# Kernel optimization log

Hardware: AMD Instinct MI355X
Metric: run time of the kernel (lower is better)

## Reference

```python
import jax, jax.numpy as jnp
import numpy as np

V, B, T, D, L, H = 32000, 2, 2048, 1024, 4, 16
HD = D // H            # 64
HID = int(2 * D * 4 / 3)  # 2730 (SwiGLU hidden, computed in BinaryMLP)
EPS = 1e-6


def setup_inputs() -> dict:
    key = jax.random.key(0)
    ks = jax.random.split(key, 16)
    s = 0.02
    return {
        'emb': jax.random.normal(ks[0], (V, D), jnp.float32) * s,
        'Wq':  jax.random.normal(ks[1], (L, D, D), jnp.float32) * s,
        'Wk':  jax.random.normal(ks[2], (L, D, D), jnp.float32) * s,
        'Wv':  jax.random.normal(ks[3], (L, D, D), jnp.float32) * s,
        'Wo':  jax.random.normal(ks[4], (L, D, D), jnp.float32) * s,
        'W1':  jax.random.normal(ks[5], (L, HID, D), jnp.float32) * s,
        'W3':  jax.random.normal(ks[6], (L, HID, D), jnp.float32) * s,
        'W2':  jax.random.normal(ks[7], (L, D, HID), jnp.float32) * s,
        'g1':  jnp.ones((L, D), jnp.float32),
        'g2':  jnp.ones((L, D), jnp.float32),
        'gf':  jnp.ones((D,), jnp.float32),
        'Wlm': jax.random.normal(ks[8], (V, D), jnp.float32) * s,
        'idx': jax.random.randint(ks[9], (B, T), 0, V, jnp.int64),
    }


def bitnet_quant(w):
    # BitNet b1.58: gamma = mean(|W|); ternarize then rescale (STE: identity grad)
    gamma = jnp.maximum(jnp.mean(jnp.abs(w)), 1e-5)
    wq = jnp.clip(jnp.round(w / gamma), -1.0, 1.0) * gamma
    return w + jax.lax.stop_gradient(wq - w)


def rmsnorm(x, g):
    return x * jax.lax.rsqrt(jnp.mean(x * x, axis=-1, keepdims=True) + EPS) * g


def rope_tables(t_len):
    inv_freq = 1.0 / (10000.0 ** (jnp.arange(0, HD, 2, dtype=jnp.float32) / HD))
    t = jnp.arange(t_len, dtype=jnp.float32)
    freqs = jnp.einsum('i,j->ij', t, inv_freq)       # [T, HD/2]
    emb = jnp.concatenate([freqs, freqs], axis=-1)    # [T, HD]
    return jnp.cos(emb), jnp.sin(emb)


def rotate_half(x):
    x1, x2 = x[..., : HD // 2], x[..., HD // 2:]
    return jnp.concatenate([-x2, x1], axis=-1)


def forward(emb, Wq, Wk, Wv, Wo, W1, W2, W3, g1, g2, gf, Wlm, idx):
    x = emb[idx]                                      # [B,T,D]
    cos, sin = rope_tables(T)                         # [T,HD]
    cos = cos[None, None]; sin = sin[None, None]      # [1,1,T,HD]
    causal = jnp.tril(jnp.ones((T, T), bool))[None, None]
    scale = 1.0 / np.sqrt(HD)

    for l in range(L):
        # --- attention ---
        h = rmsnorm(x, g1[l])
        q = jnp.einsum('btd,ed->bte', h, bitnet_quant(Wq[l]))
        k = jnp.einsum('btd,ed->bte', h, bitnet_quant(Wk[l]))
        v = jnp.einsum('btd,ed->bte', h, bitnet_quant(Wv[l]))
        q = q.reshape(B, T, H, HD).transpose(0, 2, 1, 3)  # [B,H,T,HD]
        k = k.reshape(B, T, H, HD).transpose(0, 2, 1, 3)
        v = v.reshape(B, T, H, HD).transpose(0, 2, 1, 3)
        q = q * cos + rotate_half(q) * sin
        k = k * cos + rotate_half(k) * sin
        att = jnp.einsum('bhqd,bhkd->bhqk', q, k) * scale
        att = jnp.where(causal, att, -jnp.inf)
        att = jax.nn.softmax(att, axis=-1)
        y = jnp.einsum('bhqk,bhkd->bhqd', att, v)
        y = y.transpose(0, 2, 1, 3).reshape(B, T, D)
        y = jnp.einsum('btd,ed->bte', y, bitnet_quant(Wo[l]))
        x = x + y
        # --- SwiGLU MLP ---
        h = rmsnorm(x, g2[l])
        a = jnp.einsum('btd,hd->bth', h, bitnet_quant(W1[l]))
        b = jnp.einsum('btd,hd->bth', h, bitnet_quant(W3[l]))
        m = jnp.einsum('bth,dh->btd', jax.nn.silu(a) * b, bitnet_quant(W2[l]))
        x = x + m

    x = rmsnorm(x, gf)
    logits = jnp.einsum('btd,vd->btv', x, Wlm)        # lm_head is plain Linear
    return logits


def reference(emb, Wq, Wk, Wv, Wo, W1, W2, W3, g1, g2, gf, Wlm, idx):
    return forward(emb, Wq, Wk, Wv, Wo, W1, W2, W3, g1, g2, gf, Wlm, idx)
```

## Files before the change

kernel.cpp:

```cpp
#include <hip/hip_runtime.h>

#define TT   2048
#define BBB  2
#define DDD  1024
#define LLL  4
#define HHH  16
#define VVV  32000
#define HIDR 2730
#define HIDP 2816
#define MMM  (BBB*TT)

typedef __bf16 bf16x8 __attribute__((ext_vector_type(8)));
typedef float  f32x4  __attribute__((ext_vector_type(4)));

#define BAR()    asm volatile("s_barrier" ::: "memory")
#define LGKM0()  asm volatile("s_waitcnt lgkmcnt(0)" ::: "memory")
#define VMC(n)   asm volatile("s_waitcnt vmcnt(" #n ")" ::: "memory")
#define SCHED0() __builtin_amdgcn_sched_barrier(0)

__device__ __forceinline__ void gl2lds16(const void* g, void* l) {
  __builtin_amdgcn_global_load_lds((const __attribute__((address_space(1))) void*)g,
                                   (__attribute__((address_space(3))) void*)l, 16, 0, 0);
}

__device__ __forceinline__ f32x4 mfma16(bf16x8 a, bf16x8 b, f32x4 c) {
  return __builtin_amdgcn_mfma_f32_16x16x32_bf16(a, b, c, 0, 0, 0);
}

__device__ __forceinline__ float block_reduce_sum(float v) {
  __shared__ float red[4];
  #pragma unroll
  for (int o = 32; o > 0; o >>= 1) v += __shfl_xor(v, o);
  int w = threadIdx.x >> 6;
  if ((threadIdx.x & 63) == 0) red[w] = v;
  __syncthreads();
  float r = red[0] + red[1] + red[2] + red[3];
  __syncthreads();
  return r;
}

struct QDesc { const float* src; __bf16* dst; int srcR, srcC, dstR, dstC, quant, pad_; };
struct QDescs { QDesc d[29]; };

__global__ __launch_bounds__(256) void reduce_abs_kernel(QDescs qd, float* partial) {
  const QDesc e = qd.d[blockIdx.y];
  size_t n4 = ((size_t)e.srcR * e.srcC) >> 2;
  const float4* s4 = (const float4*)e.src;
  float acc = 0.f;
  for (size_t i = (size_t)blockIdx.x * blockDim.x + threadIdx.x; i < n4;
       i += (size_t)gridDim.x * blockDim.x) {
    float4 v = s4[i];
    acc += fabsf(v.x) + fabsf(v.y) + fabsf(v.z) + fabsf(v.w);
  }
  float s = block_reduce_sum(acc);
  if (threadIdx.x == 0) partial[blockIdx.y * 256 + blockIdx.x] = s;
}

__global__ __launch_bounds__(256) void finalize_gamma_kernel(QDescs qd, const float* partial,
                                                             float* gamma) {
  int m = blockIdx.x;
  float v = partial[m * 256 + threadIdx.x];
  float s = block_reduce_sum(v);
  if (threadIdx.x == 0) {
    float n = (float)((size_t)qd.d[m].srcR * qd.d[m].srcC);
    gamma[m] = fmaxf(s / n, 1e-5f);
  }
}

__global__ __launch_bounds__(256) void quant_kernel(QDescs qd, const float* gamma) {
  const QDesc e = qd.d[blockIdx.y];
  float invg = 1.0f / gamma[blockIdx.y];
  int nc8 = e.dstC >> 3;
  for (int row = blockIdx.x; row < e.dstR; row += gridDim.x) {
    const float* srow = e.src + (size_t)row * e.srcC;
    bf16x8* drow = (bf16x8*)(e.dst + (size_t)row * e.dstC);
    bool rok = row < e.srcR;
    for (int c8 = threadIdx.x; c8 < nc8; c8 += 256) {
      int c = c8 * 8;
      float w[8];
      if (rok && c + 8 <= e.srcC) {
        float2 v01 = *(const float2*)(srow + c);
        float2 v23 = *(const float2*)(srow + c + 2);
        float2 v45 = *(const float2*)(srow + c + 4);
        float2 v67 = *(const float2*)(srow + c + 6);
        w[0] = v01.x; w[1] = v01.y; w[2] = v23.x; w[3] = v23.y;
        w[4] = v45.x; w[5] = v45.y; w[6] = v67.x; w[7] = v67.y;
      } else {
        #pragma unroll
        for (int j = 0; j < 8; ++j) w[j] = (rok && c + j < e.srcC) ? srow[c + j] : 0.f;
      }
      bf16x8 o;
      #pragma unroll
      for (int j = 0; j < 8; ++j) {
        if (e.quant) {
          float q = rintf(w[j] * invg);
          o[j] = (__bf16)fminf(1.f, fmaxf(-1.f, q));
        } else {
          o[j] = (__bf16)w[j];
        }
      }
      drow[c8] = o;
    }
  }
}

__global__ void rope_table_kernel(float* cosT, float* sinT) {
  int i = blockIdx.x * 256 + threadIdx.x;
  int t = i >> 5, j = i & 31;
  float inv = powf(10000.0f, -(float)j * (1.0f / 32.0f));
  float ang = (float)t * inv;
  cosT[i] = cosf(ang);
  sinT[i] = sinf(ang);
}

__global__ void idx_mode_kernel(const void* idxv, int* flag) {
  const long long* p = (const long long*)idxv;
  int good = 1;
  for (int i = threadIdx.x; i < (BBB * TT) / 2; i += 256) {
    long long v = p[i];
    if (v < 0 || v >= VVV) good = 0;
  }
  unsigned long long b = __ballot(good);
  __shared__ int r[4];
  if ((threadIdx.x & 63) == 0) r[threadIdx.x >> 6] = (b == ~0ULL) ? 1 : 0;
  __syncthreads();
  if (threadIdx.x == 0) flag[0] = r[0] & r[1] & r[2] & r[3];
}

__global__ __launch_bounds__(256) void gather_kernel(const float* emb, const void* idxv,
                                                     const int* flag, float* x) {
  int tok = blockIdx.x;
  long long id;
  if (flag[0]) id = ((const long long*)idxv)[tok];
  else         id = (long long)((const int*)idxv)[tok];
  const float4* src = (const float4*)(emb + (size_t)id * DDD);
  float4* dst = (float4*)(x + (size_t)tok * DDD);
  dst[threadIdx.x] = src[threadIdx.x];
}

__global__ __launch_bounds__(256) void rmsnorm_kernel(const float* x, const float* g, __bf16* h) {
  int tok = blockIdx.x;
  const float4* xr = (const float4*)(x + (size_t)tok * DDD);
  float4 v = xr[threadIdx.x];
  float ss = v.x * v.x + v.y * v.y + v.z * v.z + v.w * v.w;
  float tot = block_reduce_sum(ss);
  float r = rsqrtf(tot * (1.0f / (float)DDD) + 1e-6f);
  const float4* gr = (const float4*)g;
  float4 gv = gr[threadIdx.x];
  union { __bf16 o[4]; uint2 u2; } pk;
  pk.o[0] = (__bf16)(v.x * r * gv.x);
  pk.o[1] = (__bf16)(v.y * r * gv.y);
  pk.o[2] = (__bf16)(v.z * r * gv.z);
  pk.o[3] = (__bf16)(v.w * r * gv.w);
  *(uint2*)((char*)h + ((size_t)tok * DDD + threadIdx.x * 4) * 2) = pk.u2;
}

__global__ __launch_bounds__(256) void silumul_kernel(const __bf16* ab5, const float* gam1,
                                                      const float* gam3, __bf16* u) {
  int i = blockIdx.x * 256 + threadIdx.x;
  int row = i / (HIDP / 8);
  int c8 = i - row * (HIDP / 8);
  float g1v = gam1[0], g3v = gam3[0];
  bf16x8 av = ((const bf16x8*)ab5)[(size_t)row * (2 * HIDP / 8) + c8];
  bf16x8 bv = ((const bf16x8*)ab5)[(size_t)row * (2 * HIDP / 8) + (HIDP / 8) + c8];
  bf16x8 o;
  #pragma unroll
  for (int j = 0; j < 8; ++j) {
    float fa = (float)av[j] * g1v;
    float s = fa / (1.0f + __expf(-fa));
    o[j] = (__bf16)(s * (float)bv[j] * g3v);
  }
  ((bf16x8*)u)[i] = o;
}

__global__ __launch_bounds__(256) void repack_kernel(const __bf16* qkv, const float* cosT,
                                                     const float* sinT, __bf16* Qp, __bf16* Kp,
                                                     __bf16* Vp) {
  int bh = blockIdx.y;
  int b = bh >> 4, h = bh & 15;
  int t0 = blockIdx.x * 64;
  int r = threadIdx.x >> 2;
  int cq = (threadIdx.x & 3) * 16;
  int t = t0 + r;
  __shared__ __bf16 vt[64][72];
  size_t src = ((size_t)b * TT + t) * 3072 + h * 64;

  #pragma unroll
  for (int which = 0; which < 2; ++which) {
    const __bf16* inp = qkv + (which ? 1024 : 0);
    __bf16* outp = which ? Kp : Qp;
    __bf16 val[16], par[16];
    *(bf16x8*)&val[0] = *(const bf16x8*)(inp + src + cq);
    *(bf16x8*)&val[8] = *(const bf16x8*)(inp + src + cq + 8);
    *(bf16x8*)&par[0] = *(const bf16x8*)(inp + src + (cq ^ 32));
    *(bf16x8*)&par[8] = *(const bf16x8*)(inp + src + (cq ^ 32) + 8);
    __bf16 o[16];
    #pragma unroll
    for (int i2 = 0; i2 < 16; ++i2) {
      int d = cq + i2;
      float c = cosT[t * 32 + (d & 31)];
      float s = sinT[t * 32 + (d & 31)];
      float x0 = (float)val[i2], xp = (float)par[i2];
      float res = (d < 32) ? (x0 * c - xp * s) : (x0 * c + xp * s);
      o[i2] = (__bf16)res;
    }
    *(bf16x8*)(outp + ((size_t)bh * TT + t) * 64 + cq) = *(bf16x8*)&o[0];
    *(bf16x8*)(outp + ((size_t)bh * TT + t) * 64 + cq + 8) = *(bf16x8*)&o[8];
  }

  bf16x8 v0 = *(const bf16x8*)(qkv + 2048 + src + cq);
  bf16x8 v1 = *(const bf16x8*)(qkv + 2048 + src + cq + 8);
  #pragma unroll
  for (int i2 = 0; i2 < 8; ++i2) {
    vt[r][cq + i2] = v0[i2];
    vt[r][cq + 8 + i2] = v1[i2];
  }
  __syncthreads();
  __bf16 ov[16];
  #pragma unroll
  for (int i2 = 0; i2 < 16; ++i2) ov[i2] = vt[cq + i2][r];
  *(bf16x8*)(Vp + ((size_t)bh * 64 + r) * TT + t0 + cq) = *(bf16x8*)&ov[0];
  *(bf16x8*)(Vp + ((size_t)bh * 64 + r) * TT + t0 + cq + 8) = *(bf16x8*)&ov[8];
}

__global__ __launch_bounds__(256) void attn_kernel(const __bf16* __restrict__ Qp,
                                                   const __bf16* __restrict__ Kp,
                                                   const __bf16* __restrict__ Vp,
                                                   __bf16* __restrict__ y) {
  int nwg = gridDim.x * gridDim.y;
  int orig = blockIdx.y * gridDim.x + blockIdx.x;
  int qq = nwg >> 3;
  int swz = (orig & 7) * qq + (orig >> 3);
  int qt = swz % gridDim.x, bh = swz / gridDim.x;

  int b = bh >> 4, h = bh & 15;
  int lane = threadIdx.x & 63, wave = threadIdx.x >> 6;
  int l15 = lane & 15, l4 = lane >> 4;
  int q0 = qt * 128;
  const int ssw = (l15 & 7);
  const int csw = ((lane & 7) ^ (lane >> 3)) * 8;
  const float SC = 0.125f * 1.44269504f;

  __shared__ __bf16 Ks[2][64 * 64];
  __shared__ __bf16 Vts[2][64 * 64];
  __shared__ __bf16 Ps[4][32 * 64];

  const __bf16* Qb = Qp + (size_t)bh * TT * 64;
  bf16x8 qf[2][2];
  #pragma unroll
  for (int mf = 0; mf < 2; ++mf)
    #pragma unroll
    for (int kk = 0; kk < 2; ++kk)
      qf[mf][kk] = *(const bf16x8*)(Qb + (size_t)(q0 + wave * 32 + mf * 16 + l15) * 64 +
                                    kk * 32 + l4 * 8);

  const f32x4 z4 = {0.f, 0.f, 0.f, 0.f};
  f32x4 acc[2][4];
  float mrow[2][4], lrow[2][4];
  #pragma unroll
  for (int mf = 0; mf < 2; ++mf)
    #pragma unroll
    for (int j = 0; j < 4; ++j) { mrow[mf][j] = -1e30f; lrow[mf][j] = 0.f; }
  #pragma unroll
  for (int mf = 0; mf < 2; ++mf)
    #pragma unroll
    for (int df = 0; df < 4; ++df) acc[mf][df] = z4;

  auto stage = [&](int kt, int buf) {
    int k0 = kt * 64;
    #pragma unroll
    for (int i = 0; i < 2; ++i) {
      int rbase = wave * 16 + i * 8;
      int row = rbase + (lane >> 3);
      gl2lds16(Kp + ((size_t)bh * TT + k0 + row) * 64 + csw, &Ks[buf][rbase * 64]);
      gl2lds16(Vp + ((size_t)bh * 64 + row) * TT + k0 + csw, &Vts[buf][rbase * 64]);
    }
  };

  int nkt = q0 / 64 + 2;
  stage(0, 0);
  __syncthreads();

  for (int kt = 0; kt < nkt; ++kt) {
    int k0 = kt * 64;
    int cur = kt & 1;
    if (kt + 1 < nkt) stage(kt + 1, cur ^ 1);
    const __bf16* KsC = Ks[cur];
    const __bf16* VtsC = Vts[cur];

    f32x4 s[2][4];
    #pragma unroll
    for (int mf = 0; mf < 2; ++mf)
      #pragma unroll
      for (int nf = 0; nf < 4; ++nf) s[mf][nf] = z4;
    #pragma unroll
    for (int kk = 0; kk < 2; ++kk) {
      int slot = ((kk * 4 + l4) ^ ssw) * 8;
      bf16x8 kf[4];
      #pragma unroll
      for (int nf = 0; nf < 4; ++nf)
        kf[nf] = *(const bf16x8*)&KsC[(nf * 16 + l15) * 64 + slot];
      #pragma unroll
      for (int mf = 0; mf < 2; ++mf)
        #pragma unroll
        for (int nf = 0; nf < 4; ++nf) s[mf][nf] = mfma16(qf[mf][kk], kf[nf], s[mf][nf]);
    }

    bool domask = (k0 + 63 > q0);
    #pragma unroll
    for (int mf = 0; mf < 2; ++mf) {
      int qrowb = q0 + wave * 32 + mf * 16 + l4 * 4;
      #pragma unroll
      for (int nf = 0; nf < 4; ++nf) {
        int kg = k0 + nf * 16 + l15;
        #pragma unroll
        for (int j = 0; j < 4; ++j) {
          float vv = s[mf][nf][j] * SC;
          if (domask && kg > qrowb + j) vv = -1e30f;
          s[mf][nf][j] = vv;
        }
      }
    }

    float mx_[2][4];
    float exm = -1e30f;
    #pragma unroll
    for (int mf = 0; mf < 2; ++mf)
      #pragma unroll
      for (int j = 0; j < 4; ++j) {
        float mx = fmaxf(fmaxf(s[mf][0][j], s[mf][1][j]), fmaxf(s[mf][2][j], s[mf][3][j]));
        mx = fmaxf(mx, __shfl_xor(mx, 1));
        mx = fmaxf(mx, __shfl_xor(mx, 2));
        mx = fmaxf(mx, __shfl_xor(mx, 4));
        mx = fmaxf(mx, __shfl_xor(mx, 8));
        mx_[mf][j] = mx;
        exm = fmaxf(exm, mx - mrow[mf][j]);
      }
    if (__ballot(exm > 8.0f) != 0ULL) {
      #pragma unroll
      for (int mf = 0; mf < 2; ++mf)
        #pragma unroll
        for (int j = 0; j < 4; ++j) {
          float mnew = fmaxf(mrow[mf][j], mx_[mf][j]);
          float alpha = exp2f(mrow[mf][j] - mnew);
          mrow[mf][j] = mnew;
          lrow[mf][j] *= alpha;
          #pragma unroll
          for (int df = 0; df < 4; ++df) acc[mf][df][j] *= alpha;
        }
    }

    float psum[2][4];
    #pragma unroll
    for (int mf = 0; mf < 2; ++mf)
      #pragma unroll
      for (int j = 0; j < 4; ++j) psum[mf][j] = 0.f;
    #pragma unroll
    for (int mf = 0; mf < 2; ++mf)
      #pragma unroll
      for (int nf = 0; nf < 4; ++nf)
        #pragma unroll
        for (int j = 0; j < 4; ++j) {
          float pp = exp2f(s[mf][nf][j] - mrow[mf][j]);
          psum[mf][j] += pp;
          int prow = mf * 16 + l4 * 4 + j;
          int pcol = nf * 16 + l15;
          Ps[wave][prow * 64 + (pcol ^ ((prow & 7) << 3))] = (__bf16)pp;
        }
    #pragma unroll
    for (int mf = 0; mf < 2; ++mf)
      #pragma unroll
      for (int j = 0; j < 4; ++j) {
        float rs = psum[mf][j];
        rs += __shfl_xor(rs, 1);
        rs += __shfl_xor(rs, 2);
        rs += __shfl_xor(rs, 4);
        rs += __shfl_xor(rs, 8);
        lrow[mf][j] += rs;
      }

    #pragma unroll
    for (int kk = 0; kk < 2; ++kk) {
      int slot = ((kk * 4 + l4) ^ ssw) * 8;
      bf16x8 pf[2], vf[4];
      #pragma unroll
      for (int mf = 0; mf < 2; ++mf)
        pf[mf] = *(const bf16x8*)&Ps[wave][(mf * 16 + l15) * 64 + slot];
      #pragma unroll
      for (int df = 0; df < 4; ++df)
        vf[df] = *(const bf16x8*)&VtsC[(df * 16 + l15) * 64 + slot];
      #pragma unroll
      for (int mf = 0; mf < 2; ++mf)
        #pragma unroll
        for (int df = 0; df < 4; ++df) acc[mf][df] = mfma16(pf[mf], vf[df], acc[mf][df]);
    }
    __syncthreads();
  }

  #pragma unroll
  for (int mf = 0; mf < 2; ++mf)
    #pragma unroll
    for (int j = 0; j < 4; ++j) {
      float inv = 1.0f / lrow[mf][j];
      int qg = q0 + wave * 32 + mf * 16 + l4 * 4 + j;
      size_t base = ((size_t)b * TT + qg) * DDD + h * 64;
      #pragma unroll
      for (int df = 0; df < 4; ++df)
        y[base + df * 16 + l15] = (__bf16)(acc[mf][df][j] * inv);
    }
}

template <int MODE>
__global__ __launch_bounds__(256) void gemm_kernel(const __bf16* __restrict__ A,
                                                   const __bf16* __restrict__ Bw, void* Cout,
                                                   const float* Res, const float* gscale,
                                                   int gshift, int M, int N, int K) {
  __shared__ __bf16 As[128 * 64];
  __shared__ __bf16 Bs[128 * 64];
  int nwg = gridDim.x * gridDim.y;
  int orig = blockIdx.y * gridDim.x + blockIdx.x;
  int qq = nwg >> 3;
  int swz = (orig & 7) * qq + (orig >> 3);
  int bx = swz % gridDim.x, by = swz / gridDim.x;
  const int m0 = bx * 128, n0 = by * 128;

  const int lane = threadIdx.x & 63, wave = threadIdx.x >> 6;
  const int wr = wave >> 1, wc = wave & 1;
  const int l15 = lane & 15, l4 = lane >> 4;
  const int ssw = (l15 & 7);
  const int csw = ((lane & 7) ^ (lane >> 3)) * 8;
  const f32x4 z4 = {0.f, 0.f, 0.f, 0.f};
  f32x4 acc[4][4];
  #pragma unroll
  for (int i = 0; i < 4; ++i)
    #pragma unroll
    for (int j = 0; j < 4; ++j) acc[i][j] = z4;

  const int nk = K >> 6;
  for (int kt = 0; kt < nk; ++kt) {
    const int kb = kt << 6;
    #pragma unroll
    for (int i = 0; i < 4; ++i) {
      int rbase = wave * 32 + i * 8;
      int row = rbase + (lane >> 3);
      gl2lds16(A + (size_t)(m0 + row) * K + kb + csw, &As[rbase * 64]);
      gl2lds16(Bw + (size_t)(n0 + row) * K + kb + csw, &Bs[rbase * 64]);
    }
    __syncthreads();
    #pragma unroll
    for (int kk = 0; kk < 2; ++kk) {
      int slot = ((kk * 4 + l4) ^ ssw) * 8;
      bf16x8 af[4], bfr[4];
      #pragma unroll
      for (int mi = 0; mi < 4; ++mi)
        af[mi] = *(const bf16x8*)&As[(wr * 64 + mi * 16 + l15) * 64 + slot];
      #pragma unroll
      for (int ni = 0; ni < 4; ++ni)
        bfr[ni] = *(const bf16x8*)&Bs[(wc * 64 + ni * 16 + l15) * 64 + slot];
      #pragma unroll
      for (int mi = 0; mi < 4; ++mi)
        #pragma unroll
        for (int ni = 0; ni < 4; ++ni) acc[mi][ni] = mfma16(af[mi], bfr[ni], acc[mi][ni]);
    }
    __syncthreads();
  }

  float sc = gscale ? gscale[n0 >> gshift] : 1.0f;
  #pragma unroll
  for (int mi = 0; mi < 4; ++mi)
    #pragma unroll
    for (int ni = 0; ni < 4; ++ni)
      #pragma unroll
      for (int j = 0; j < 4; ++j) {
        int r = m0 + wr * 64 + mi * 16 + l4 * 4 + j;
        int c = n0 + wc * 64 + ni * 16 + l15;
        size_t off = (size_t)r * N + c;
        float v = acc[mi][ni][j] * sc;
        if (MODE == 0) ((__bf16*)Cout)[off] = (__bf16)v;
        else if (MODE == 1) ((float*)Cout)[off] = Res[off] + v;
        else ((float*)Cout)[off] = v;
      }
}

template <int MODE>
__global__ __launch_bounds__(512, 2) void gemm256_kernel(const __bf16* __restrict__ A,
                                                         const __bf16* __restrict__ Bw,
                                                         void* Cout, const float* Res,
                                                         const float* gscale, int gshift,
                                                         int M, int N, int K) {
  __shared__ __bf16 AS[2][2][256 * 32];
  __shared__ __bf16 BS[2][2][256 * 32];
  int nwg = gridDim.x * gridDim.y;
  int orig = blockIdx.y * gridDim.x + blockIdx.x;
  int qq = nwg >> 3;
  int swz = (orig & 7) * qq + (orig >> 3);
  int bx = swz % gridDim.x, by = swz / gridDim.x;
  const int m0 = bx * 256, n0 = by * 256;

  const int tid = threadIdx.x;
  const int lane = tid & 63, w = tid >> 6;
  const int wr = w >> 2, wc = w & 3;
  const int l15 = lane & 15, l4 = lane >> 4;
  const int lsw = (l15 >> 1) & 3;
  const int srow = w * 16 + (lane >> 2);
  const int sslot = ((lane & 3) ^ ((lane >> 3) & 3)) * 8;

  f32x4 acc[8][4];
  const f32x4 z4 = {0.f, 0.f, 0.f, 0.f};
  #pragma unroll
  for (int i = 0; i < 8; ++i)
    #pragma unroll
    for (int j = 0; j < 4; ++j) acc[i][j] = z4;

  auto stageA = [&](int b, int kh, int t) {
    const __bf16* g = A + (size_t)(m0 + srow) * K + (size_t)t * 64 + kh * 32 + sslot;
    gl2lds16(g, &AS[b][kh][w * 512]);
    gl2lds16(g + (size_t)128 * K, &AS[b][kh][4096 + w * 512]);
  };
  auto stageB = [&](int b, int kh, int t) {
    const __bf16* g = Bw + (size_t)(n0 + srow) * K + (size_t)t * 64 + kh * 32 + sslot;
    gl2lds16(g, &BS[b][kh][w * 512]);
    gl2lds16(g + (size_t)128 * K, &BS[b][kh][4096 + w * 512]);
  };

  bf16x8 af[4], bq[4];
  auto ldA = [&](int b, int kh, int mh) {
    #pragma unroll
    for (int mi = 0; mi < 4; ++mi) {
      int row = wr * 128 + (mh * 4 + mi) * 16 + l15;
      af[mi] = *(const bf16x8*)&AS[b][kh][row * 32 + ((l4 ^ lsw) * 8)];
    }
  };
  auto ldB = [&](int b, int kh) {
    #pragma unroll
    for (int ni = 0; ni < 4; ++ni) {
      int row = wc * 64 + ni * 16 + l15;
      bq[ni] = *(const bf16x8*)&BS[b][kh][row * 32 + ((l4 ^ lsw) * 8)];
    }
  };
  auto domfma = [&](int mh) {
    __builtin_amdgcn_s_setprio(1);
    #pragma unroll
    for (int mi = 0; mi < 4; ++mi)
      #pragma unroll
      for (int ni = 0; ni < 4; ++ni)
        acc[mh * 4 + mi][ni] = mfma16(af[mi], bq[ni], acc[mh * 4 + mi][ni]);
    __builtin_amdgcn_s_setprio(0);
  };

  const int nk = K >> 6;
  const int niter = nk >> 1;
  stageA(0, 0, 0); stageB(0, 0, 0); stageA(0, 1, 0); stageB(0, 1, 0);
  stageB(1, 0, 1); stageA(1, 0, 1); stageB(1, 1, 1);
  VMC(6); SCHED0();
  BAR();

  for (int j = 0; j < niter; ++j) {
    int t1 = 2 * j + 1;
    int t2 = 2 * j + 2; if (t2 > nk - 1) t2 = nk - 1;
    int t3 = 2 * j + 3; if (t3 > nk - 1) t3 = nk - 1;
    ldB(0, 0); ldA(0, 0, 0);
    stageA(1, 1, t1);
    BAR(); LGKM0(); SCHED0();
    domfma(0);
    BAR();
    ldA(0, 0, 1);
    stageB(0, 0, t2);
    BAR(); LGKM0(); SCHED0();
    domfma(1);
    BAR();
    ldB(0, 1); ldA(0, 1, 0);
    stageA(0, 0, t2);
    BAR(); LGKM0(); SCHED0();
    domfma(0);
    BAR();
    ldA(0, 1, 1);
    VMC(4); SCHED0();
    stageB(0, 1, t2);
    BAR(); LGKM0(); SCHED0();
    domfma(1);
    BAR();
    ldB(1, 0); ldA(1, 0, 0);
    stageA(0, 1, t2);
    BAR(); LGKM0(); SCHED0();
    domfma(0);
    BAR();
    ldA(1, 0, 1);
    stageB(1, 0, t3);
    BAR(); LGKM0(); SCHED0();
    domfma(1);
    BAR();
    ldB(1, 1); ldA(1, 1, 0);
    stageA(1, 0, t3);
    BAR(); LGKM0(); SCHED0();
    domfma(0);
    BAR();
    ldA(1, 1, 1);
    VMC(4); SCHED0();
    stageB(1, 1, t3);
    BAR(); LGKM0(); SCHED0();
    domfma(1);
    BAR();
  }

  float sc = gscale ? gscale[n0 >> gshift] : 1.0f;
  #pragma unroll
  for (int mi = 0; mi < 8; ++mi)
    #pragma unroll
    for (int ni = 0; ni < 4; ++ni)
      #pragma unroll
      for (int j = 0; j < 4; ++j) {
        int r = m0 + wr * 128 + mi * 16 + l4 * 4 + j;
        int c = n0 + wc * 64 + ni * 16 + l15;
        size_t off = (size_t)r * N + c;
        float v = acc[mi][ni][j] * sc;
        if (MODE == 0) ((__bf16*)Cout)[off] = (__bf16)v;
        else if (MODE == 1) ((float*)Cout)[off] = Res[off] + v;
        else ((float*)Cout)[off] = v;
      }
}

extern "C" void kernel_launch(void* const* d_in, const int* in_sizes, int n_in,
                              void* d_out, int out_size, void* d_ws, size_t ws_size,
                              hipStream_t stream) {
  (void)in_sizes; (void)n_in; (void)out_size; (void)ws_size;
  const float* emb = (const float*)d_in[0];
  const float* Wq  = (const float*)d_in[1];
  const float* Wk  = (const float*)d_in[2];
  const float* Wv  = (const float*)d_in[3];
  const float* Wo  = (const float*)d_in[4];
  const float* W1  = (const float*)d_in[5];
  const float* W3  = (const float*)d_in[6];
  const float* W2  = (const float*)d_in[7];
  const float* g1  = (const float*)d_in[8];
  const float* g2  = (const float*)d_in[9];
  const float* gf  = (const float*)d_in[10];
  const float* Wlm = (const float*)d_in[11];
  const void*  idx = d_in[12];
  float* out = (float*)d_out;

  char* p = (char*)d_ws;
  auto take = [&](size_t bytes) -> char* {
    char* r = p;
    p += (bytes + 255) & ~(size_t)255;
    return r;
  };
  __bf16* WqkvQ = (__bf16*)take((size_t)LLL * 3072 * DDD * 2);
  __bf16* WoQ  = (__bf16*)take((size_t)LLL * DDD * DDD * 2);
  __bf16* W13Q = (__bf16*)take((size_t)LLL * 2 * HIDP * DDD * 2);
  __bf16* W2Q  = (__bf16*)take((size_t)LLL * DDD * HIDP * 2);
  __bf16* WlmB = (__bf16*)take((size_t)VVV * DDD * 2);
  float*  xbuf = (float*)take((size_t)MMM * DDD * 4);
  __bf16* hbuf = (__bf16*)take((size_t)MMM * DDD * 2);
  char*   S    = take(69206016);
  float*  cosT = (float*)take((size_t)TT * 32 * 4);
  float*  sinT = (float*)take((size_t)TT * 32 * 4);
  float*  gamma = (float*)take(128);
  float*  partial = (float*)take(29 * 256 * 4);
  int*    flag = (int*)take(256);

  __bf16* qkv = (__bf16*)(S);
  __bf16* Qp  = (__bf16*)(S + 25165824);
  __bf16* Kp  = (__bf16*)(S + 33554432);
  __bf16* Vp  = (__bf16*)(S + 41943040);
  __bf16* ab5 = (__bf16*)(S);
  __bf16* ub  = (__bf16*)(S + 46137344);

  QDescs qd;
  for (int l = 0; l < LLL; ++l) {
    qd.d[l * 4 + 0] = QDesc{Wq + (size_t)l * DDD * DDD,
                            WqkvQ + (size_t)l * 3072 * DDD, DDD, DDD, DDD, DDD, 1, 0};
    qd.d[l * 4 + 1] = QDesc{Wk + (size_t)l * DDD * DDD,
                            WqkvQ + (size_t)l * 3072 * DDD + (size_t)DDD * DDD,
                            DDD, DDD, DDD, DDD, 1, 0};
    qd.d[l * 4 + 2] = QDesc{Wv + (size_t)l * DDD * DDD,
                            WqkvQ + (size_t)l * 3072 * DDD + (size_t)2 * DDD * DDD,
                            DDD, DDD, DDD, DDD, 1, 0};
    qd.d[l * 4 + 3] = QDesc{Wo + (size_t)l * DDD * DDD, WoQ + (size_t)l * DDD * DDD,
                            DDD, DDD, DDD, DDD, 1, 0};
    qd.d[16 + l] = QDesc{W1 + (size_t)l * HIDR * DDD,
                         W13Q + (size_t)l * 2 * HIDP * DDD,
                         HIDR, DDD, HIDP, DDD, 1, 0};
    qd.d[20 + l] = QDesc{W3 + (size_t)l * HIDR * DDD,
                         W13Q + (size_t)l * 2 * HIDP * DDD + (size_t)HIDP * DDD,
                         HIDR, DDD, HIDP, DDD, 1, 0};
    qd.d[24 + l] = QDesc{W2 + (size_t)l * DDD * HIDR, W2Q + (size_t)l * DDD * HIDP,
                         DDD, HIDR, DDD, HIDP, 1, 0};
  }
  qd.d[28] = QDesc{Wlm, WlmB, VVV, DDD, VVV, DDD, 0, 0};

  reduce_abs_kernel<<<dim3(256, 28), 256, 0, stream>>>(qd, partial);
  finalize_gamma_kernel<<<28, 256, 0, stream>>>(qd, partial, gamma);
  quant_kernel<<<dim3(512, 29), 256, 0, stream>>>(qd, gamma);
  rope_table_kernel<<<(TT * 32) / 256, 256, 0, stream>>>(cosT, sinT);
  idx_mode_kernel<<<1, 256, 0, stream>>>(idx, flag);
  gather_kernel<<<MMM, 256, 0, stream>>>(emb, idx, flag, xbuf);

  for (int l = 0; l < LLL; ++l) {
    rmsnorm_kernel<<<MMM, 256, 0, stream>>>(xbuf, g1 + (size_t)l * DDD, hbuf);
    gemm256_kernel<0><<<dim3(16, 12), 512, 0, stream>>>(
        hbuf, WqkvQ + (size_t)l * 3072 * DDD, qkv, nullptr, gamma + l * 4, 10,
        MMM, 3072, DDD);
    repack_kernel<<<dim3(TT / 64, BBB * HHH), 256, 0, stream>>>(qkv, cosT, sinT, Qp, Kp, Vp);
    attn_kernel<<<dim3(TT / 128, BBB * HHH), 256, 0, stream>>>(Qp, Kp, Vp, hbuf);
    gemm_kernel<1><<<dim3(32, 8), 256, 0, stream>>>(hbuf, WoQ + (size_t)l * DDD * DDD, xbuf,
                                                    xbuf, gamma + l * 4 + 3, 30, MMM, DDD, DDD);
    rmsnorm_kernel<<<MMM, 256, 0, stream>>>(xbuf, g2 + (size_t)l * DDD, hbuf);
    gemm256_kernel<0><<<dim3(16, 2 * HIDP / 256), 512, 0, stream>>>(
        hbuf, W13Q + (size_t)l * 2 * HIDP * DDD, ab5, nullptr, nullptr, 30,
        MMM, 2 * HIDP, DDD);
    silumul_kernel<<<(MMM * HIDP / 8) / 256, 256, 0, stream>>>(ab5, gamma + 16 + l,
                                                               gamma + 20 + l, ub);
    gemm_kernel<1><<<dim3(32, 8), 256, 0, stream>>>(ub, W2Q + (size_t)l * DDD * HIDP, xbuf,
                                                    xbuf, gamma + 24 + l, 30, MMM, DDD, HIDP);
  }
  rmsnorm_kernel<<<MMM, 256, 0, stream>>>(xbuf, gf, hbuf);
  gemm256_kernel<2><<<dim3(16, VVV / 256), 512, 0, stream>>>(hbuf, WlmB, out, nullptr, nullptr,
                                                             30, MMM, VVV, DDD);
}
```

Before: 2.001 ms.

## Fuse SiLU-gate into W1/W3 GEMM epilogue via row-interleaved weights; add MFMA priority hints

```diff
diff --git a/kernel.cpp b/kernel.cpp
--- a/kernel.cpp
+++ b/kernel.cpp
@@ -39,7 +39,7 @@
   return r;
 }
 
-struct QDesc { const float* src; __bf16* dst; int srcR, srcC, dstR, dstC, quant, pad_; };
+struct QDesc { const float* src; __bf16* dst; int srcR, srcC, dstR, dstC, quant, rmul; };
 struct QDescs { QDesc d[29]; };
 
 __global__ __launch_bounds__(256) void reduce_abs_kernel(QDescs qd, float* partial) {
@@ -73,7 +73,7 @@
   int nc8 = e.dstC >> 3;
   for (int row = blockIdx.x; row < e.dstR; row += gridDim.x) {
     const float* srow = e.src + (size_t)row * e.srcC;
-    bf16x8* drow = (bf16x8*)(e.dst + (size_t)row * e.dstC);
+    bf16x8* drow = (bf16x8*)(e.dst + (size_t)row * e.rmul * e.dstC);
     bool rok = row < e.srcR;
     for (int c8 = threadIdx.x; c8 < nc8; c8 += 256) {
       int c = c8 * 8;
@@ -155,24 +155,6 @@
   *(uint2*)((char*)h + ((size_t)tok * DDD + threadIdx.x * 4) * 2) = pk.u2;
 }
 
-__global__ __launch_bounds__(256) void silumul_kernel(const __bf16* ab5, const float* gam1,
-                                                      const float* gam3, __bf16* u) {
-  int i = blockIdx.x * 256 + threadIdx.x;
-  int row = i / (HIDP / 8);
-  int c8 = i - row * (HIDP / 8);
-  float g1v = gam1[0], g3v = gam3[0];
-  bf16x8 av = ((const bf16x8*)ab5)[(size_t)row * (2 * HIDP / 8) + c8];
-  bf16x8 bv = ((const bf16x8*)ab5)[(size_t)row * (2 * HIDP / 8) + (HIDP / 8) + c8];
-  bf16x8 o;
-  #pragma unroll
-  for (int j = 0; j < 8; ++j) {
-    float fa = (float)av[j] * g1v;
-    float s = fa / (1.0f + __expf(-fa));
-    o[j] = (__bf16)(s * (float)bv[j] * g3v);
-  }
-  ((bf16x8*)u)[i] = o;
-}
-
 __global__ __launch_bounds__(256) void repack_kernel(const __bf16* qkv, const float* cosT,
                                                      const float* sinT, __bf16* Qp, __bf16* Kp,
                                                      __bf16* Vp) {
@@ -293,6 +275,7 @@
     for (int mf = 0; mf < 2; ++mf)
       #pragma unroll
       for (int nf = 0; nf < 4; ++nf) s[mf][nf] = z4;
+    __builtin_amdgcn_s_setprio(1);
     #pragma unroll
     for (int kk = 0; kk < 2; ++kk) {
       int slot = ((kk * 4 + l4) ^ ssw) * 8;
@@ -305,6 +288,7 @@
         #pragma unroll
         for (int nf = 0; nf < 4; ++nf) s[mf][nf] = mfma16(qf[mf][kk], kf[nf], s[mf][nf]);
     }
+    __builtin_amdgcn_s_setprio(0);
 
     bool domask = (k0 + 63 > q0);
     #pragma unroll
@@ -379,6 +363,7 @@
         lrow[mf][j] += rs;
       }
 
+    __builtin_amdgcn_s_setprio(1);
     #pragma unroll
     for (int kk = 0; kk < 2; ++kk) {
       int slot = ((kk * 4 + l4) ^ ssw) * 8;
@@ -394,6 +379,7 @@
         #pragma unroll
         for (int df = 0; df < 4; ++df) acc[mf][df] = mfma16(pf[mf], vf[df], acc[mf][df]);
     }
+    __builtin_amdgcn_s_setprio(0);
     __syncthreads();
   }
 
@@ -603,6 +589,31 @@
     BAR();
   }
 
+  if (MODE == 3) {
+    float g1v = gscale[0], g3v = gscale[4];
+    __bf16* U = (__bf16*)Cout;
+    int half = N >> 1;
+    #pragma unroll
+    for (int mi = 0; mi < 8; ++mi)
+      #pragma unroll
+      for (int ni = 0; ni < 4; ++ni)
+        #pragma unroll
+        for (int j = 0; j < 4; ++j) {
+          int r = m0 + wr * 128 + mi * 16 + l4 * 4 + j;
+          int c = n0 + wc * 64 + ni * 16 + l15;
+          float v = acc[mi][ni][j];
+          float av = v * g1v;
+          float bv = v * g3v;
+          float pav = __shfl_xor(av, 1);
+          float pbv = __shfl_xor(bv, 1);
+          float aa = (lane & 1) ? pav : av;
+          float bb = (lane & 1) ? bv : pbv;
+          float u = aa / (1.0f + __expf(-aa)) * bb;
+          if (!(lane & 1)) U[(size_t)r * half + (c >> 1)] = (__bf16)u;
+        }
+    return;
+  }
+
   float sc = gscale ? gscale[n0 >> gshift] : 1.0f;
   #pragma unroll
   for (int mi = 0; mi < 8; ++mi)
@@ -663,31 +674,30 @@
   __bf16* Qp  = (__bf16*)(S + 25165824);
   __bf16* Kp  = (__bf16*)(S + 33554432);
   __bf16* Vp  = (__bf16*)(S + 41943040);
-  __bf16* ab5 = (__bf16*)(S);
   __bf16* ub  = (__bf16*)(S + 46137344);
 
   QDescs qd;
   for (int l = 0; l < LLL; ++l) {
     qd.d[l * 4 + 0] = QDesc{Wq + (size_t)l * DDD * DDD,
-                            WqkvQ + (size_t)l * 3072 * DDD, DDD, DDD, DDD, DDD, 1, 0};
+                            WqkvQ + (size_t)l * 3072 * DDD, DDD, DDD, DDD, DDD, 1, 1};
     qd.d[l * 4 + 1] = QDesc{Wk + (size_t)l * DDD * DDD,
                             WqkvQ + (size_t)l * 3072 * DDD + (size_t)DDD * DDD,
-                            DDD, DDD, DDD, DDD, 1, 0};
+                            DDD, DDD, DDD, DDD, 1, 1};
     qd.d[l * 4 + 2] = QDesc{Wv + (size_t)l * DDD * DDD,
                             WqkvQ + (size_t)l * 3072 * DDD + (size_t)2 * DDD * DDD,
-                            DDD, DDD, DDD, DDD, 1, 0};
+                            DDD, DDD, DDD, DDD, 1, 1};
     qd.d[l * 4 + 3] = QDesc{Wo + (size_t)l * DDD * DDD, WoQ + (size_t)l * DDD * DDD,
-                            DDD, DDD, DDD, DDD, 1, 0};
+                            DDD, DDD, DDD, DDD, 1, 1};
     qd.d[16 + l] = QDesc{W1 + (size_t)l * HIDR * DDD,
                          W13Q + (size_t)l * 2 * HIDP * DDD,
-                         HIDR, DDD, HIDP, DDD, 1, 0};
+                         HIDR, DDD, HIDP, DDD, 1, 2};
     qd.d[20 + l] = QDesc{W3 + (size_t)l * HIDR * DDD,
-                         W13Q + (size_t)l * 2 * HIDP * DDD + (size_t)HIDP * DDD,
-                         HIDR, DDD, HIDP, DDD, 1, 0};
+                         W13Q + (size_t)l * 2 * HIDP * DDD + (size_t)DDD,
+                         HIDR, DDD, HIDP, DDD, 1, 2};
     qd.d[24 + l] = QDesc{W2 + (size_t)l * DDD * HIDR, W2Q + (size_t)l * DDD * HIDP,
-                         DDD, HIDR, DDD, HIDP, 1, 0};
-  }
-  qd.d[28] = QDesc{Wlm, WlmB, VVV, DDD, VVV, DDD, 0, 0};
+                         DDD, HIDR, DDD, HIDP, 1, 1};
+  }
+  qd.d[28] = QDesc{Wlm, WlmB, VVV, DDD, VVV, DDD, 0, 1};
 
   reduce_abs_kernel<<<dim3(256, 28), 256, 0, stream>>>(qd, partial);
   finalize_gamma_kernel<<<28, 256, 0, stream>>>(qd, partial, gamma);
@@ -706,11 +716,9 @@
     gemm_kernel<1><<<dim3(32, 8), 256, 0, stream>>>(hbuf, WoQ + (size_t)l * DDD * DDD, xbuf,
                                                     xbuf, gamma + l * 4 + 3, 30, MMM, DDD, DDD);
     rmsnorm_kernel<<<MMM, 256, 0, stream>>>(xbuf, g2 + (size_t)l * DDD, hbuf);
-    gemm256_kernel<0><<<dim3(16, 2 * HIDP / 256), 512, 0, stream>>>(
-        hbuf, W13Q + (size_t)l * 2 * HIDP * DDD, ab5, nullptr, nullptr, 30,
+    gemm256_kernel<3><<<dim3(16, 2 * HIDP / 256), 512, 0, stream>>>(
+        hbuf, W13Q + (size_t)l * 2 * HIDP * DDD, ub, nullptr, gamma + 16 + l, 30,
         MMM, 2 * HIDP, DDD);
-    silumul_kernel<<<(MMM * HIDP / 8) / 256, 256, 0, stream>>>(ab5, gamma + 16 + l,
-                                                               gamma + 20 + l, ub);
     gemm_kernel<1><<<dim3(32, 8), 256, 0, stream>>>(ub, W2Q + (size_t)l * DDD * HIDP, xbuf,
                                                     xbuf, gamma + 24 + l, 30, MMM, DDD, HIDP);
   }
```

Result: no change. 2.007 ms (+0.3%).
